# Optimization experiments

Hardware: AMD Instinct MI355X
Metric: run time of the kernel (lower is better)

## Reference

```python
import jax, jax.numpy as jnp
import numpy as np

B, T, DM, D, W, DG = 2, 4096, 2048, 4096, 4, 512  # batch, seq, model hidden, conv channels (value_dim), kernel size, generator hidden


def setup_inputs() -> dict:
    key = jax.random.key(0)
    k0, k1, k2, k3, k4 = jax.random.split(key, 5)
    return {
        "x": jax.random.normal(k0, (B, T, D), jnp.float32) * 0.02,
        "generator_input": jax.random.normal(k1, (B, T, DM), jnp.float32) * 0.02,
        "w1": jax.random.normal(k2, (DG, DM), jnp.float32) * 0.02,   # Linear(DM -> DG), no bias
        "w2": jax.random.normal(k3, (D * W, DG), jnp.float32) * 0.02,  # Linear(DG -> D*W)
        "b2": jax.random.normal(k4, (D * W,), jnp.float32) * 0.02,
    }


def reference(x, generator_input, w1, w2, b2):
    # Hypernetwork: per-token depthwise conv kernels [B, T, D, W]
    h = jax.nn.silu(jnp.einsum("btm,gm->btg", generator_input, w1))
    kflat = jnp.einsum("btg,kg->btk", h, w2) + b2
    kernels = kflat.reshape(x.shape[0], x.shape[1], x.shape[2], W)
    # Causal depthwise conv: left-pad by W-1, windowed multiply-accumulate.
    xp = jnp.pad(x, ((0, 0), (W - 1, 0), (0, 0)))
    Tlen = x.shape[1]
    y = kernels[..., 0] * xp[:, 0:Tlen, :]
    for w in range(1, W):
        y = y + kernels[..., w] * xp[:, w:w + Tlen, :]
    return jax.nn.silu(y)  # [B, T, D]
```

## Files before the change

kernel.cpp:

```cpp
#include <hip/hip_runtime.h>
#include <hip/hip_bf16.h>
#include <stdint.h>

#define TLEN 4096
#define DMm  2048
#define DD   4096
#define DGg  512
#define BT   8192
#define DW   16384

typedef __attribute__((ext_vector_type(8))) short bf16x8;
typedef __attribute__((ext_vector_type(4))) float f32x4;

__device__ __forceinline__ unsigned short f2bf(float f) {
    union { float f; unsigned u; } c; c.f = f;
    unsigned u = c.u;
    unsigned r = (u + 0x7FFFu + ((u >> 16) & 1u)) >> 16;
    return (unsigned short)r;
}

#define NB1 (BT * DMm / 4)
#define NB2 (DGg * DMm / 4)
#define NB3 (DW * DGg / 4)
__global__ void cast_all_kernel(const float* __restrict__ g,
                                const float* __restrict__ w1,
                                const float* __restrict__ w2,
                                unsigned short* __restrict__ o) {
    int i = blockIdx.x * blockDim.x + threadIdx.x;
    if (i >= NB1 + NB2 + NB3) return;
    const float* src; int j = i;
    if (j < NB1) { src = g; }
    else if (j < NB1 + NB2) { src = w1; j -= NB1; }
    else { src = w2; j -= NB1 + NB2; }
    float4 v = reinterpret_cast<const float4*>(src)[j];
    ushort4 u;
    u.x = f2bf(v.x); u.y = f2bf(v.y); u.z = f2bf(v.z); u.w = f2bf(v.w);
    reinterpret_cast<ushort4*>(o)[i] = u;
}

#define GLDS16(gp, lp)                                                         \
    __builtin_amdgcn_global_load_lds(                                          \
        (__attribute__((address_space(1))) const void*)(gp),                   \
        (__attribute__((address_space(3))) void*)(lp), 16, 0, 0)

#define VMCNT(n) asm volatile("s_waitcnt vmcnt(" #n ")" ::: "memory")
#define SBAR()   __builtin_amdgcn_s_barrier()
#define SCHED0() __builtin_amdgcn_sched_barrier(0)

__global__ __launch_bounds__(256) void gemm1_silu_kernel(
    const unsigned short* __restrict__ A,
    const unsigned short* __restrict__ Bm,
    unsigned short* __restrict__ H)
{
    __shared__ short smA[128 * 32];
    __shared__ short smB[128 * 32];
    const int m0   = blockIdx.y * 128;
    const int n0   = blockIdx.x * 128;
    const int lane = threadIdx.x & 63;
    const int wave = threadIdx.x >> 6;
    const int wm   = wave >> 1, wn = wave & 1;

    const int c0 = wave * 64 + lane;
    const int c1 = c0 + 256;
    const int rA0 = m0 + (c0 >> 2), rA1 = m0 + (c1 >> 2);
    const int rB0 = n0 + (c0 >> 2), rB1 = n0 + (c1 >> 2);
    const int ko0 = (c0 & 3) * 8,  ko1 = (c1 & 3) * 8;

    f32x4 acc[4][4] = {};

    for (int k0 = 0; k0 < DMm; k0 += 32) {
        GLDS16(A  + (size_t)rA0 * DMm + k0 + ko0, smA + wave * 512);
        GLDS16(A  + (size_t)rA1 * DMm + k0 + ko1, smA + 2048 + wave * 512);
        GLDS16(Bm + (size_t)rB0 * DMm + k0 + ko0, smB + wave * 512);
        GLDS16(Bm + (size_t)rB1 * DMm + k0 + ko1, smB + 2048 + wave * 512);
        __syncthreads();

        const int la = lane & 15, ko = (lane >> 4) * 8;
        bf16x8 af[4], bfr[4];
#pragma unroll
        for (int mm = 0; mm < 4; ++mm)
            af[mm] = *reinterpret_cast<const bf16x8*>(&smA[(wm * 64 + mm * 16 + la) * 32 + ko]);
#pragma unroll
        for (int nn = 0; nn < 4; ++nn)
            bfr[nn] = *reinterpret_cast<const bf16x8*>(&smB[(wn * 64 + nn * 16 + la) * 32 + ko]);
#pragma unroll
        for (int mm = 0; mm < 4; ++mm)
#pragma unroll
            for (int nn = 0; nn < 4; ++nn)
                acc[mm][nn] = __builtin_amdgcn_mfma_f32_16x16x32_bf16(
                    af[mm], bfr[nn], acc[mm][nn], 0, 0, 0);
        __syncthreads();
    }

#pragma unroll
    for (int mm = 0; mm < 4; ++mm) {
        int rowB = m0 + wm * 64 + mm * 16 + (lane >> 4) * 4;
#pragma unroll
        for (int nn = 0; nn < 4; ++nn) {
            int colG = n0 + wn * 64 + nn * 16 + (lane & 15);
#pragma unroll
            for (int j = 0; j < 4; ++j) {
                float v = acc[mm][nn][j];
                float s = v / (1.0f + __expf(-v));
                H[(size_t)(rowB + j) * DGg + colG] = f2bf(s);
            }
        }
    }
}

#define LDS_B2 49152

__global__ __launch_bounds__(512, 4) void gemm2_conv_silu_kernel(
    const unsigned short* __restrict__ Hb,
    const unsigned short* __restrict__ W2b,
    const float* __restrict__ b2,
    const float* __restrict__ x,
    float* __restrict__ out)
{
    __shared__ __attribute__((aligned(16))) char lds[73728];
    const int tid  = threadIdx.x;
    const int lane = tid & 63, wave = tid >> 6;
    const int wm   = wave >> 1, wn = wave & 1;
    const int la   = lane & 15, hi = lane >> 4;

    int bid = blockIdx.x;
    int swz = (bid & 7) * 512 + (bid >> 3);
    const int n0 = (swz >> 6) * 256;
    const int t0 = (swz & 63) * 128;
    const int d0 = n0 >> 2;

    const int srow = lane >> 2;
    const int scol = ((lane & 3) ^ ((srow >> 1) & 3)) * 8;

    auto stageA = [&](int tk, int p) {
#pragma unroll
        for (int q = 0; q < 2; ++q) {
            int chunk = wave * 2 + q, row = chunk * 16 + srow;
            GLDS16(W2b + (size_t)(n0 + row) * DGg + tk * 32 + scol,
                   lds + p * 16384 + chunk * 1024);
        }
    };
    auto stageB = [&](int tk, int p) {
        int row = wave * 16 + srow;
        GLDS16(Hb + (size_t)(t0 + row) * DGg + tk * 32 + scol,
               lds + LDS_B2 + p * 8192 + wave * 1024);
    };

    f32x4 acc[4][4] = {};
    const int slotb = (hi ^ ((la >> 1) & 3)) * 16;
    const int aOff  = (wm * 64 + la) * 64 + slotb;
    const int bOff  = LDS_B2 + (wn * 64 + la) * 64 + slotb;

    auto region = [&](int r, bool doStage) {
        const int p = r % 3;
        const char* aB = lds + p * 16384 + aOff;
        const char* bB = lds + p * 8192 + bOff;
        bf16x8 aF[4], bF[4];
#pragma unroll
        for (int m = 0; m < 4; ++m)
            aF[m] = *reinterpret_cast<const bf16x8*>(aB + m * 1024);
#pragma unroll
        for (int nr = 0; nr < 4; ++nr)
            bF[nr] = *reinterpret_cast<const bf16x8*>(bB + nr * 1024);
        if (doStage) { stageA(r + 2, (r + 2) % 3); stageB(r + 2, (r + 2) % 3); }
        SCHED0();
        __builtin_amdgcn_s_setprio(1);
#pragma unroll
        for (int m = 0; m < 4; ++m)
#pragma unroll
            for (int nr = 0; nr < 4; ++nr)
                acc[m][nr] = __builtin_amdgcn_mfma_f32_16x16x32_bf16(
                    aF[m], bF[nr], acc[m][nr], 0, 0, 0);
        __builtin_amdgcn_s_setprio(0);
        SCHED0();
    };

    stageA(0, 0); stageB(0, 0);
    stageA(1, 1); stageB(1, 1);
    VMCNT(3);
    SBAR();

#pragma unroll
    for (int r = 0; r < 14; ++r) {
        region(r, true);
        VMCNT(3);
        SBAR();
    }
    region(14, false); VMCNT(0); SBAR();
    region(15, false);

    float4 xv[5];
#pragma unroll
    for (int k = 0; k < 5; ++k) {
        int c = tid + k * 512;
        float4 v = make_float4(0.f, 0.f, 0.f, 0.f);
        if (c < 2096) {
            int row = c >> 4, q = c & 15;
            int rg = t0 - 3 + row;
            if (rg >= 0 && (rg >> 12) == (t0 >> 12))
                v = *reinterpret_cast<const float4*>(&x[(size_t)rg * DD + d0 + q * 4]);
        }
        xv[k] = v;
    }
    __syncthreads();

    float* smX = reinterpret_cast<float*>(lds);
#pragma unroll
    for (int k = 0; k < 5; ++k) {
        int c = tid + k * 512;
        if (c < 2096) {
            int row = c >> 4, q = c & 15;
            *reinterpret_cast<float4*>(&smX[row * 68 + q * 4]) = xv[k];
        }
    }
    __syncthreads();

    float4 bb[4];
#pragma unroll
    for (int m = 0; m < 4; ++m)
        bb[m] = *reinterpret_cast<const float4*>(&b2[n0 + wm * 64 + m * 16 + hi * 4]);

    float* smY = reinterpret_cast<float*>(lds + 35632);
#pragma unroll
    for (int nr = 0; nr < 4; ++nr) {
        int tl = wn * 64 + nr * 16 + la;
#pragma unroll
        for (int m = 0; m < 4; ++m) {
            int dl = wm * 16 + m * 4 + hi;
            float pv =
                  (acc[m][nr][0] + bb[m].x) * smX[(tl + 0) * 68 + dl]
                + (acc[m][nr][1] + bb[m].y) * smX[(tl + 1) * 68 + dl]
                + (acc[m][nr][2] + bb[m].z) * smX[(tl + 2) * 68 + dl]
                + (acc[m][nr][3] + bb[m].w) * smX[(tl + 3) * 68 + dl];
            smY[tl * 68 + dl] = pv / (1.0f + __expf(-pv));
        }
    }
    __syncthreads();

    for (int c = tid; c < 128 * 16; c += 512) {
        int row = c >> 4, q = c & 15;
        float4 v = *reinterpret_cast<const float4*>(&smY[row * 68 + q * 4]);
        *reinterpret_cast<float4*>(&out[(size_t)(t0 + row) * DD + d0 + q * 4]) = v;
    }
}

extern "C" void kernel_launch(void* const* d_in, const int* in_sizes, int n_in,
                              void* d_out, int out_size, void* d_ws, size_t ws_size,
                              hipStream_t stream) {
    const float* x   = (const float*)d_in[0];
    const float* gen = (const float*)d_in[1];
    const float* w1  = (const float*)d_in[2];
    const float* w2  = (const float*)d_in[3];
    const float* b2  = (const float*)d_in[4];
    float* out = (float*)d_out;

    char* ws = (char*)d_ws;
    size_t off = 0;
    unsigned short* gen_b = (unsigned short*)(ws + off); off += (size_t)BT * DMm * 2;
    unsigned short* w1_b  = (unsigned short*)(ws + off); off += (size_t)DGg * DMm * 2;
    unsigned short* w2_b  = (unsigned short*)(ws + off); off += (size_t)DW * DGg * 2;
    unsigned short* h_b   = (unsigned short*)(ws + off); off += (size_t)BT * DGg * 2;

    int total4 = NB1 + NB2 + NB3;
    cast_all_kernel<<<(total4 + 255) / 256, 256, 0, stream>>>(gen, w1, w2, gen_b);

    gemm1_silu_kernel<<<dim3(DGg / 128, BT / 128), 256, 0, stream>>>(gen_b, w1_b, h_b);
    gemm2_conv_silu_kernel<<<4096, 512, 0, stream>>>(h_b, w2_b, b2, x, out);
}
```

Before: 237.2 us.

## Load W2 fragments directly into registers and deepen H LDS pipeline

The second GEMM now reads its W2 operand straight from global memory into double-buffered registers instead of staging it through LDS. Only the H tile is still staged in LDS, with a 4-deep ring in place of the old 3-deep one. This removes LDS traffic and footprint for the A operand and lets more H stages be in flight. In exchange each lane issues uncoalesced 16-byte global loads for W2 and holds more live registers, which may hurt occupancy under launch_bounds(512,4).

```diff
diff --git a/kernel.cpp b/kernel.cpp
--- a/kernel.cpp
+++ b/kernel.cpp
@@ -108,7 +108,7 @@
     }
 }
 
-#define LDS_B2 49152
+#define XSTR2 68
 
 __global__ __launch_bounds__(512, 4) void gemm2_conv_silu_kernel(
     const unsigned short* __restrict__ Hb,
@@ -117,7 +117,7 @@
     const float* __restrict__ x,
     float* __restrict__ out)
 {
-    __shared__ __attribute__((aligned(16))) char lds[73728];
+    __shared__ __attribute__((aligned(16))) char lds[70448];
     const int tid  = threadIdx.x;
     const int lane = tid & 63, wave = tid >> 6;
     const int wm   = wave >> 1, wn = wave & 1;
@@ -132,37 +132,34 @@
     const int srow = lane >> 2;
     const int scol = ((lane & 3) ^ ((srow >> 1) & 3)) * 8;
 
-    auto stageA = [&](int tk, int p) {
-#pragma unroll
-        for (int q = 0; q < 2; ++q) {
-            int chunk = wave * 2 + q, row = chunk * 16 + srow;
-            GLDS16(W2b + (size_t)(n0 + row) * DGg + tk * 32 + scol,
-                   lds + p * 16384 + chunk * 1024);
-        }
-    };
     auto stageB = [&](int tk, int p) {
         int row = wave * 16 + srow;
         GLDS16(Hb + (size_t)(t0 + row) * DGg + tk * 32 + scol,
-               lds + LDS_B2 + p * 8192 + wave * 1024);
+               lds + p * 8192 + wave * 1024);
+    };
+
+    const unsigned short* aBase = W2b + (size_t)(n0 + wm * 64 + la) * DGg + hi * 8;
+    auto loadA = [&](bf16x8 (&dst)[4], int tk) {
+#pragma unroll
+        for (int m = 0; m < 4; ++m)
+            dst[m] = *reinterpret_cast<const bf16x8*>(aBase + (size_t)m * 16 * DGg + tk * 32);
     };
 
     f32x4 acc[4][4] = {};
     const int slotb = (hi ^ ((la >> 1) & 3)) * 16;
-    const int aOff  = (wm * 64 + la) * 64 + slotb;
-    const int bOff  = LDS_B2 + (wn * 64 + la) * 64 + slotb;
-
-    auto region = [&](int r, bool doStage) {
-        const int p = r % 3;
-        const char* aB = lds + p * 16384 + aOff;
+    const int bOff  = (wn * 64 + la) * 64 + slotb;
+
+    bf16x8 aF0[4], aF1[4];
+
+    auto body = [&](bf16x8 (&AC)[4], bf16x8 (&AN)[4], int p, int tkA, bool doA,
+                    int tkB, bool doB) {
+        bf16x8 bF[4];
         const char* bB = lds + p * 8192 + bOff;
-        bf16x8 aF[4], bF[4];
-#pragma unroll
-        for (int m = 0; m < 4; ++m)
-            aF[m] = *reinterpret_cast<const bf16x8*>(aB + m * 1024);
 #pragma unroll
         for (int nr = 0; nr < 4; ++nr)
             bF[nr] = *reinterpret_cast<const bf16x8*>(bB + nr * 1024);
-        if (doStage) { stageA(r + 2, (r + 2) % 3); stageB(r + 2, (r + 2) % 3); }
+        if (doA) loadA(AN, tkA);
+        if (doB) stageB(tkB, tkB & 3);
         SCHED0();
         __builtin_amdgcn_s_setprio(1);
 #pragma unroll
@@ -170,24 +167,27 @@
 #pragma unroll
             for (int nr = 0; nr < 4; ++nr)
                 acc[m][nr] = __builtin_amdgcn_mfma_f32_16x16x32_bf16(
-                    aF[m], bF[nr], acc[m][nr], 0, 0, 0);
+                    AC[m], bF[nr], acc[m][nr], 0, 0, 0);
         __builtin_amdgcn_s_setprio(0);
         SCHED0();
     };
 
-    stageA(0, 0); stageB(0, 0);
-    stageA(1, 1); stageB(1, 1);
-    VMCNT(3);
+    loadA(aF0, 0);
+    stageB(0, 0); stageB(1, 1); stageB(2, 2);
+    VMCNT(2);
     SBAR();
 
-#pragma unroll
-    for (int r = 0; r < 14; ++r) {
-        region(r, true);
-        VMCNT(3);
+    body(aF0, aF1, 0, 1, true, 3, true);  VMCNT(6); SBAR();
+#pragma unroll
+    for (int r = 1; r <= 12; ++r) {
+        if (r & 1) body(aF1, aF0, r & 3, r + 1, true, r + 3, true);
+        else       body(aF0, aF1, r & 3, r + 1, true, r + 3, true);
+        VMCNT(6);
         SBAR();
     }
-    region(14, false); VMCNT(0); SBAR();
-    region(15, false);
+    body(aF1, aF0, 1, 14, true, 0, false); VMCNT(5); SBAR();
+    body(aF0, aF1, 2, 15, true, 0, false); VMCNT(4); SBAR();
+    body(aF1, aF0, 3, 0, false, 0, false);
 
     float4 xv[5];
 #pragma unroll
@@ -210,7 +210,7 @@
         int c = tid + k * 512;
         if (c < 2096) {
             int row = c >> 4, q = c & 15;
-            *reinterpret_cast<float4*>(&smX[row * 68 + q * 4]) = xv[k];
+            *reinterpret_cast<float4*>(&smX[row * XSTR2 + q * 4]) = xv[k];
         }
     }
     __syncthreads();
@@ -228,18 +228,18 @@
         for (int m = 0; m < 4; ++m) {
             int dl = wm * 16 + m * 4 + hi;
             float pv =
-                  (acc[m][nr][0] + bb[m].x) * smX[(tl + 0) * 68 + dl]
-                + (acc[m][nr][1] + bb[m].y) * smX[(tl + 1) * 68 + dl]
-                + (acc[m][nr][2] + bb[m].z) * smX[(tl + 2) * 68 + dl]
-                + (acc[m][nr][3] + bb[m].w) * smX[(tl + 3) * 68 + dl];
-            smY[tl * 68 + dl] = pv / (1.0f + __expf(-pv));
+                  (acc[m][nr][0] + bb[m].x) * smX[(tl + 0) * XSTR2 + dl]
+                + (acc[m][nr][1] + bb[m].y) * smX[(tl + 1) * XSTR2 + dl]
+                + (acc[m][nr][2] + bb[m].z) * smX[(tl + 2) * XSTR2 + dl]
+                + (acc[m][nr][3] + bb[m].w) * smX[(tl + 3) * XSTR2 + dl];
+            smY[tl * XSTR2 + dl] = pv / (1.0f + __expf(-pv));
         }
     }
     __syncthreads();
 
     for (int c = tid; c < 128 * 16; c += 512) {
         int row = c >> 4, q = c & 15;
-        float4 v = *reinterpret_cast<const float4*>(&smY[row * 68 + q * 4]);
+        float4 v = *reinterpret_cast<const float4*>(&smY[row * XSTR2 + q * 4]);
         *reinterpret_cast<float4*>(&out[(size_t)(t0 + row) * DD + d0 + q * 4]) = v;
     }
 }
```

Result: slower. 355.2 us (+49.8%).

## Pipeline gemm1 with triple-buffered LDS, swizzled tiles, and coalesced epilogue

Applied to the files above, without the earlier changes.

Rewrites the first GEMM (generator input times w1, then SiLU) as a 64x128 tile kernel. It uses a three-stage global-to-LDS prefetch pipeline with a single barrier per k-step, an XOR-swizzled LDS layout to reduce bank conflicts, and a block-index swizzle for L2 locality. The epilogue now stages results through LDS so it can write H with 16-byte stores instead of scattered 2-byte stores. The aim is to hide load latency and remove the two syncthreads per k-step. In exchange the tiles are smaller, so each block does less MFMA work per byte loaded, and the pipeline bookkeeping is more complex.

```diff
diff --git a/kernel.cpp b/kernel.cpp
--- a/kernel.cpp
+++ b/kernel.cpp
@@ -47,64 +47,105 @@
 #define SBAR()   __builtin_amdgcn_s_barrier()
 #define SCHED0() __builtin_amdgcn_sched_barrier(0)
 
-__global__ __launch_bounds__(256) void gemm1_silu_kernel(
-    const unsigned short* __restrict__ A,
-    const unsigned short* __restrict__ Bm,
+#define G1_B 12288
+
+__global__ __launch_bounds__(256, 2) void gemm1_silu_kernel(
+    const unsigned short* __restrict__ Gen_b,
+    const unsigned short* __restrict__ W1b,
     unsigned short* __restrict__ H)
 {
-    __shared__ short smA[128 * 32];
-    __shared__ short smB[128 * 32];
-    const int m0   = blockIdx.y * 128;
-    const int n0   = blockIdx.x * 128;
-    const int lane = threadIdx.x & 63;
-    const int wave = threadIdx.x >> 6;
+    __shared__ __attribute__((aligned(16))) char lds[36864];
+    const int tid  = threadIdx.x;
+    const int lane = tid & 63, wave = tid >> 6;
     const int wm   = wave >> 1, wn = wave & 1;
-
-    const int c0 = wave * 64 + lane;
-    const int c1 = c0 + 256;
-    const int rA0 = m0 + (c0 >> 2), rA1 = m0 + (c1 >> 2);
-    const int rB0 = n0 + (c0 >> 2), rB1 = n0 + (c1 >> 2);
-    const int ko0 = (c0 & 3) * 8,  ko1 = (c1 & 3) * 8;
-
-    f32x4 acc[4][4] = {};
-
-    for (int k0 = 0; k0 < DMm; k0 += 32) {
-        GLDS16(A  + (size_t)rA0 * DMm + k0 + ko0, smA + wave * 512);
-        GLDS16(A  + (size_t)rA1 * DMm + k0 + ko1, smA + 2048 + wave * 512);
-        GLDS16(Bm + (size_t)rB0 * DMm + k0 + ko0, smB + wave * 512);
-        GLDS16(Bm + (size_t)rB1 * DMm + k0 + ko1, smB + 2048 + wave * 512);
-        __syncthreads();
-
-        const int la = lane & 15, ko = (lane >> 4) * 8;
-        bf16x8 af[4], bfr[4];
-#pragma unroll
-        for (int mm = 0; mm < 4; ++mm)
-            af[mm] = *reinterpret_cast<const bf16x8*>(&smA[(wm * 64 + mm * 16 + la) * 32 + ko]);
-#pragma unroll
-        for (int nn = 0; nn < 4; ++nn)
-            bfr[nn] = *reinterpret_cast<const bf16x8*>(&smB[(wn * 64 + nn * 16 + la) * 32 + ko]);
-#pragma unroll
-        for (int mm = 0; mm < 4; ++mm)
-#pragma unroll
-            for (int nn = 0; nn < 4; ++nn)
-                acc[mm][nn] = __builtin_amdgcn_mfma_f32_16x16x32_bf16(
-                    af[mm], bfr[nn], acc[mm][nn], 0, 0, 0);
-        __syncthreads();
-    }
-
-#pragma unroll
-    for (int mm = 0; mm < 4; ++mm) {
-        int rowB = m0 + wm * 64 + mm * 16 + (lane >> 4) * 4;
-#pragma unroll
-        for (int nn = 0; nn < 4; ++nn) {
-            int colG = n0 + wn * 64 + nn * 16 + (lane & 15);
+    const int la   = lane & 15, hi = lane >> 4;
+
+    int bid = blockIdx.x;
+    int swz = (bid & 7) * 64 + (bid >> 3);
+    const int g0 = (swz & 7) * 64;
+    const int t0 = (swz >> 3) * 128;
+
+    const int srow = lane >> 2;
+    const int scol = ((lane & 3) ^ ((srow >> 1) & 3)) * 8;
+
+    auto stageA = [&](int tk, int p) {
+        int row = wave * 16 + srow;
+        GLDS16(W1b + (size_t)(g0 + row) * DMm + tk * 32 + scol,
+               lds + p * 4096 + wave * 1024);
+    };
+    auto stageB = [&](int tk, int p) {
+#pragma unroll
+        for (int q = 0; q < 2; ++q) {
+            int chunk = wave * 2 + q, row = chunk * 16 + srow;
+            GLDS16(Gen_b + (size_t)(t0 + row) * DMm + tk * 32 + scol,
+                   lds + G1_B + p * 8192 + chunk * 1024);
+        }
+    };
+
+    f32x4 acc[2][4] = {};
+    const int slotb = (hi ^ ((la >> 1) & 3)) * 16;
+    const int aOff  = (wm * 32 + la) * 64 + slotb;
+    const int bOff  = G1_B + (wn * 64 + la) * 64 + slotb;
+
+    auto region = [&](int r, bool doStage) {
+        const int p = r % 3;
+        const char* aB = lds + p * 4096 + aOff;
+        const char* bB = lds + p * 8192 + bOff;
+        bf16x8 aF[2], bF[4];
+#pragma unroll
+        for (int m = 0; m < 2; ++m)
+            aF[m] = *reinterpret_cast<const bf16x8*>(aB + m * 1024);
+#pragma unroll
+        for (int nr = 0; nr < 4; ++nr)
+            bF[nr] = *reinterpret_cast<const bf16x8*>(bB + nr * 1024);
+        if (doStage) { stageA(r + 2, (r + 2) % 3); stageB(r + 2, (r + 2) % 3); }
+        SCHED0();
+        __builtin_amdgcn_s_setprio(1);
+#pragma unroll
+        for (int m = 0; m < 2; ++m)
+#pragma unroll
+            for (int nr = 0; nr < 4; ++nr)
+                acc[m][nr] = __builtin_amdgcn_mfma_f32_16x16x32_bf16(
+                    aF[m], bF[nr], acc[m][nr], 0, 0, 0);
+        __builtin_amdgcn_s_setprio(0);
+        SCHED0();
+    };
+
+    stageA(0, 0); stageB(0, 0);
+    stageA(1, 1); stageB(1, 1);
+    VMCNT(3);
+    SBAR();
+
+    for (int r = 0; r < 62; ++r) {
+        region(r, true);
+        VMCNT(3);
+        SBAR();
+    }
+    region(62, false); VMCNT(0); SBAR();
+    region(63, false);
+
+    __syncthreads();
+
+    unsigned short* smY = reinterpret_cast<unsigned short*>(lds);
+#pragma unroll
+    for (int nr = 0; nr < 4; ++nr) {
+        int tl = wn * 64 + nr * 16 + la;
+#pragma unroll
+        for (int m = 0; m < 2; ++m) {
+            int gl0 = wm * 32 + m * 16 + hi * 4;
 #pragma unroll
             for (int j = 0; j < 4; ++j) {
-                float v = acc[mm][nn][j];
-                float s = v / (1.0f + __expf(-v));
-                H[(size_t)(rowB + j) * DGg + colG] = f2bf(s);
+                float v = acc[m][nr][j];
+                smY[tl * 72 + gl0 + j] = f2bf(v / (1.0f + __expf(-v)));
             }
         }
+    }
+    __syncthreads();
+
+    for (int c = tid; c < 128 * 8; c += 256) {
+        int row = c >> 3, q = c & 7;
+        bf16x8 v = *reinterpret_cast<const bf16x8*>(&smY[row * 72 + q * 8]);
+        *reinterpret_cast<bf16x8*>(&H[(size_t)(t0 + row) * DGg + g0 + q * 8]) = v;
     }
 }
 
@@ -264,6 +305,6 @@
     int total4 = NB1 + NB2 + NB3;
     cast_all_kernel<<<(total4 + 255) / 256, 256, 0, stream>>>(gen, w1, w2, gen_b);
 
-    gemm1_silu_kernel<<<dim3(DGg / 128, BT / 128), 256, 0, stream>>>(gen_b, w1_b, h_b);
+    gemm1_silu_kernel<<<512, 256, 0, stream>>>(gen_b, w1_b, h_b);
     gemm2_conv_silu_kernel<<<4096, 512, 0, stream>>>(h_b, w2_b, b2, x, out);
 }
```

Result: no change. 232.8 us (-1.9%).
